# Optimization experiments

Hardware: AMD Instinct MI355X
Metric: run time of the kernel (lower is better)

## Reference

```python
import jax, jax.numpy as jnp
import numpy as np


def setup_inputs() -> dict:
    key = jax.random.key(0)
    k1, k2 = jax.random.split(key)
    B, H, W, C, S = 128, 32, 32, 64, 64
    x = jax.random.normal(k1, (B, H, W, C), dtype=jnp.float32)
    # accumulators are positive linear-space weights (log is taken in forward)
    accumulators = jax.random.uniform(k2, (H, W, C, S), dtype=jnp.float32, minval=1e-4, maxval=1.0)
    return {"x": x, "accumulators": accumulators}


def reference(x, accumulators):
    # x: [B, H, W, C]; accumulators: [H, W, C, S] (positive, linear space)
    log_w = jnp.log(accumulators)
    # normalize weights over the input-channel axis (axis=2), per scope & sum
    log_w = jax.nn.log_softmax(log_w, axis=2)  # [H, W, C, S]
    # stable per-scope log-domain matmul: log(exp(x) @ exp(log_w))
    mx = jnp.max(x, axis=-1, keepdims=True)        # [B, H, W, 1]
    mw = jnp.max(log_w, axis=2)                    # [H, W, S]
    prod = jnp.einsum("bhwc,hwcs->bhws", jnp.exp(x - mx), jnp.exp(log_w - mw[:, :, None, :]))
    out = jnp.log(prod) + mx + mw                  # [B, H, W, S]
    return out
```

## Files before the change

### kernel.cpp

```cpp
#include <hip/hip_runtime.h>


typedef __attribute__((ext_vector_type(8))) short s8v;
typedef __attribute__((ext_vector_type(4))) float f4v;

__device__ __forceinline__ unsigned short f2bf(float f) {
    unsigned int u = __float_as_uint(f);
    u += 0x7FFFu + ((u >> 16) & 1u);
    return (unsigned short)(u >> 16);
}

__global__ __launch_bounds__(256) void sls_kernel(
    const float* __restrict__ x,
    const float* __restrict__ acc,
    float* __restrict__ out)
{
    const int hw   = blockIdx.x;
    const int bh   = blockIdx.y;
    const int t    = threadIdx.x;
    const int lane = t & 63;
    const int quad = lane >> 4;
    const int nn   = lane & 15;
    const int wave = t >> 6;

    __shared__ unsigned short e_lds[64 * 72];

    const int r0 = t >> 4;
    const int c0 = (t & 15) * 4;
    const float* xbase = x + (size_t)(bh * 64) * 65536 + (size_t)hw * 64 + c0;
    float4 xv[4];
    #pragma unroll
    for (int it = 0; it < 4; ++it)
        xv[it] = *(const float4*)(xbase + (size_t)(r0 + 16 * it) * 65536);

    const int ni = wave;
    const float* accb = acc + (size_t)hw * 4096 + ni * 16 + nn;
    float bv[2][8];
    #pragma unroll
    for (int ks = 0; ks < 2; ++ks)
        #pragma unroll
        for (int j = 0; j < 8; ++j)
            bv[ks][j] = accb[(ks * 32 + quad * 8 + j) * 64];

    #pragma unroll
    for (int it = 0; it < 4; ++it) {
        float4 v = xv[it];
        const int row = r0 + 16 * it;
        ushort4 pk;
        pk.x = f2bf(__expf(v.x));
        pk.y = f2bf(__expf(v.y));
        pk.z = f2bf(__expf(v.z));
        pk.w = f2bf(__expf(v.w));
        *(ushort4*)&e_lds[row * 72 + c0] = pk;
    }

    float csum = 0.f;
    #pragma unroll
    for (int ks = 0; ks < 2; ++ks)
        #pragma unroll
        for (int j = 0; j < 8; ++j) csum += bv[ks][j];
    csum += __shfl_xor(csum, 16);
    csum += __shfl_xor(csum, 32);
    const float lsum_n = __logf(csum);

    s8v bf0, bf1;
    #pragma unroll
    for (int j = 0; j < 8; ++j) {
        bf0[j] = (short)f2bf(bv[0][j]);
        bf1[j] = (short)f2bf(bv[1][j]);
    }

    __syncthreads();

    float* outp = out + (size_t)(bh * 64) * 65536 + (size_t)hw * 64 + ni * 16 + nn;
    #pragma unroll
    for (int mi = 0; mi < 4; ++mi) {
        const unsigned short* rowp = &e_lds[(mi * 16 + nn) * 72];
        s8v a0 = *(const s8v*)(rowp + quad * 8);
        s8v a1 = *(const s8v*)(rowp + 32 + quad * 8);
        f4v d = {0.f, 0.f, 0.f, 0.f};
        d = __builtin_amdgcn_mfma_f32_16x16x32_bf16(a0, bf0, d, 0, 0, 0);
        d = __builtin_amdgcn_mfma_f32_16x16x32_bf16(a1, bf1, d, 0, 0, 0);
        #pragma unroll
        for (int r = 0; r < 4; ++r) {
            const int b_row = mi * 16 + quad * 4 + r;
            outp[(size_t)b_row * 65536] = __logf(d[r]) - lsum_n;
        }
    }
}

extern "C" void kernel_launch(void* const* d_in, const int* in_sizes, int n_in,
                              void* d_out, int out_size, void* d_ws, size_t ws_size,
                              hipStream_t stream) {
    const float* x   = (const float*)d_in[0];
    const float* acc = (const float*)d_in[1];
    float* out = (float*)d_out;
    (void)in_sizes; (void)n_in; (void)d_ws; (void)ws_size; (void)out_size;
    sls_kernel<<<dim3(1024, 2), dim3(256), 0, stream>>>(x, acc, out);
}
```

Measured before the change: 98.96 us.

## Process both batch halves per block to reuse weights and use nontemporal memory ops

Each block now covers all 128 batch rows instead of 64. The grid drops from 1024x2 to 1024 blocks, so the accumulator column for each scope is loaded, summed and converted to bf16 once rather than twice. The second half's x tile is prefetched into registers before the first half's exp, LDS write and MFMA run, using a double-buffered LDS array. Loads of x and stores of out become nontemporal to avoid polluting cache with streaming data. The costs are fewer blocks in flight (less parallelism across CUs) and more registers per thread.

```diff
diff --git a/kernel.cpp b/kernel.cpp
--- a/kernel.cpp
+++ b/kernel.cpp
@@ -16,22 +16,22 @@
     float* __restrict__ out)
 {
     const int hw   = blockIdx.x;
-    const int bh   = blockIdx.y;
     const int t    = threadIdx.x;
     const int lane = t & 63;
     const int quad = lane >> 4;
     const int nn   = lane & 15;
     const int wave = t >> 6;
 
-    __shared__ unsigned short e_lds[64 * 72];
+    __shared__ unsigned short e_lds[2][64 * 72];
 
     const int r0 = t >> 4;
     const int c0 = (t & 15) * 4;
-    const float* xbase = x + (size_t)(bh * 64) * 65536 + (size_t)hw * 64 + c0;
-    float4 xv[4];
+    const float* xbase = x + (size_t)hw * 64 + c0;
+
+    f4v xv0[4], xv1[4];
     #pragma unroll
     for (int it = 0; it < 4; ++it)
-        xv[it] = *(const float4*)(xbase + (size_t)(r0 + 16 * it) * 65536);
+        xv0[it] = __builtin_nontemporal_load((const f4v*)(xbase + (size_t)(r0 + 16 * it) * 65536));
 
     const int ni = wave;
     const float* accb = acc + (size_t)hw * 4096 + ni * 16 + nn;
@@ -43,15 +43,19 @@
             bv[ks][j] = accb[(ks * 32 + quad * 8 + j) * 64];
 
     #pragma unroll
+    for (int it = 0; it < 4; ++it)
+        xv1[it] = __builtin_nontemporal_load((const f4v*)(xbase + (size_t)(64 + r0 + 16 * it) * 65536));
+
+    #pragma unroll
     for (int it = 0; it < 4; ++it) {
-        float4 v = xv[it];
+        f4v v = xv0[it];
         const int row = r0 + 16 * it;
         ushort4 pk;
         pk.x = f2bf(__expf(v.x));
         pk.y = f2bf(__expf(v.y));
         pk.z = f2bf(__expf(v.z));
         pk.w = f2bf(__expf(v.w));
-        *(ushort4*)&e_lds[row * 72 + c0] = pk;
+        *(ushort4*)&e_lds[0][row * 72 + c0] = pk;
     }
 
     float csum = 0.f;
@@ -72,10 +76,10 @@
 
     __syncthreads();
 
-    float* outp = out + (size_t)(bh * 64) * 65536 + (size_t)hw * 64 + ni * 16 + nn;
+    float* outp = out + (size_t)hw * 64 + ni * 16 + nn;
     #pragma unroll
     for (int mi = 0; mi < 4; ++mi) {
-        const unsigned short* rowp = &e_lds[(mi * 16 + nn) * 72];
+        const unsigned short* rowp = &e_lds[0][(mi * 16 + nn) * 72];
         s8v a0 = *(const s8v*)(rowp + quad * 8);
         s8v a1 = *(const s8v*)(rowp + 32 + quad * 8);
         f4v d = {0.f, 0.f, 0.f, 0.f};
@@ -84,7 +88,35 @@
         #pragma unroll
         for (int r = 0; r < 4; ++r) {
             const int b_row = mi * 16 + quad * 4 + r;
-            outp[(size_t)b_row * 65536] = __logf(d[r]) - lsum_n;
+            __builtin_nontemporal_store(__logf(d[r]) - lsum_n, outp + (size_t)b_row * 65536);
+        }
+    }
+
+    #pragma unroll
+    for (int it = 0; it < 4; ++it) {
+        f4v v = xv1[it];
+        const int row = r0 + 16 * it;
+        ushort4 pk;
+        pk.x = f2bf(__expf(v.x));
+        pk.y = f2bf(__expf(v.y));
+        pk.z = f2bf(__expf(v.z));
+        pk.w = f2bf(__expf(v.w));
+        *(ushort4*)&e_lds[1][row * 72 + c0] = pk;
+    }
+    __syncthreads();
+
+    #pragma unroll
+    for (int mi = 0; mi < 4; ++mi) {
+        const unsigned short* rowp = &e_lds[1][(mi * 16 + nn) * 72];
+        s8v a0 = *(const s8v*)(rowp + quad * 8);
+        s8v a1 = *(const s8v*)(rowp + 32 + quad * 8);
+        f4v d = {0.f, 0.f, 0.f, 0.f};
+        d = __builtin_amdgcn_mfma_f32_16x16x32_bf16(a0, bf0, d, 0, 0, 0);
+        d = __builtin_amdgcn_mfma_f32_16x16x32_bf16(a1, bf1, d, 0, 0, 0);
+        #pragma unroll
+        for (int r = 0; r < 4; ++r) {
+            const int b_row = 64 + mi * 16 + quad * 4 + r;
+            __builtin_nontemporal_store(__logf(d[r]) - lsum_n, outp + (size_t)b_row * 65536);
         }
     }
 }
@@ -96,5 +128,5 @@
     const float* acc = (const float*)d_in[1];
     float* out = (float*)d_out;
     (void)in_sizes; (void)n_in; (void)d_ws; (void)ws_size; (void)out_size;
-    sls_kernel<<<dim3(1024, 2), dim3(256), 0, stream>>>(x, acc, out);
+    sls_kernel<<<dim3(1024), dim3(256), 0, stream>>>(x, acc, out);
 }
```

After: 98.71 us. Within noise of the previous version (-0.3%).
